# Kernel tuning notes

Measured on AMD Instinct MI355X. Metric: run time of the kernel, lower is better.

The kernel has to match this reference:

```python
import jax, jax.numpy as jnp
import numpy as np

B, N, C, H = 4, 1024, 1024, 16
D = C // H  # head_dim = 64


def _xavier(key, shape, gain):
    fan_in, fan_out = shape[1], shape[0]
    limit = gain * np.sqrt(6.0 / (fan_in + fan_out))
    return jax.random.uniform(key, shape, jnp.float32, -limit, limit)


def setup_inputs() -> dict:
    key = jax.random.key(0)
    ks = jax.random.split(key, 12)
    g = 2.0 ** (-0.5)
    return {
        "x": jax.random.normal(ks[0], (B, N, C), jnp.float32),
        "attn_bias": jax.random.normal(ks[1], (B, H, N, N), jnp.float32),
        "attn_mask": jnp.ones((B, N), jnp.int32),
        "Wq": _xavier(ks[2], (C, C), g), "bq": jnp.zeros((C,), jnp.float32),
        "Wk": _xavier(ks[3], (C, C), g), "bk": jnp.zeros((C,), jnp.float32),
        "Wv": _xavier(ks[4], (C, C), g), "bv": jnp.zeros((C,), jnp.float32),
        "Wo": _xavier(ks[5], (C, C), 1.0), "bo": jnp.zeros((C,), jnp.float32),
    }


def reference(x, attn_bias, attn_mask, Wq, bq, Wk, bk, Wv, bv, Wo, bo):
    scale = D ** (-0.5)
    # projections; nn.Linear computes x @ W.T + b
    def proj(W, b):
        return (x @ W.T + b).reshape(B, N, H, D).transpose(0, 2, 1, 3)  # [B,H,N,D]
    q = proj(Wq, bq) * scale
    k = proj(Wk, bk)
    v = proj(Wv, bv)
    scores = jnp.einsum("bhnd,bhmd->bhnm", q, k)  # [B,H,N,N]
    scores = scores + attn_bias  # attn_bias_type == 'add'
    # 2D mask [B,N] -> [B,1,1,N]; masked_fill where mask == 0
    mask = attn_mask[:, None, None, :]
    scores = jnp.where(mask == 0, -jnp.inf, scores)
    weights = jax.nn.softmax(scores, axis=-1)  # stable (internal max subtract)
    # attn_drop is identity in eval / p=0.0
    out = jnp.einsum("bhnm,bhmd->bhnd", weights, v)
    out = out.transpose(0, 2, 1, 3).reshape(B, N, C)
    return out @ Wo.T + bo
```

## Files before the change

kernel.cpp:

```cpp
#include <hip/hip_runtime.h>
#include <hip/hip_bf16.h>

#define B_ 4
#define N_ 1024
#define C_ 1024
#define H_ 16
#define D_ 64

typedef __attribute__((ext_vector_type(8))) short bf16x8;
typedef __attribute__((ext_vector_type(4))) float f32x4;

__device__ __forceinline__ void gld_lds16(const void* g, void* l) {
    __builtin_amdgcn_global_load_lds(
        (const __attribute__((address_space(1))) void*)g,
        (__attribute__((address_space(3))) void*)l, 16, 0, 0);
}

__global__ __launch_bounds__(256) void f2b_kernel(const float* __restrict__ s,
                                                  __hip_bfloat16* __restrict__ d,
                                                  int n) {
    int i = (blockIdx.x * 256 + threadIdx.x) * 4;
    if (i < n) {
        float4 v = *(const float4*)&s[i];
        d[i + 0] = __float2bfloat16(v.x);
        d[i + 1] = __float2bfloat16(v.y);
        d[i + 2] = __float2bfloat16(v.z);
        d[i + 3] = __float2bfloat16(v.w);
    }
}

__global__ __launch_bounds__(256) void f2b4_kernel(const float* __restrict__ w0,
                                                   const float* __restrict__ w1,
                                                   const float* __restrict__ w2,
                                                   const float* __restrict__ w3,
                                                   __hip_bfloat16* __restrict__ d0,
                                                   __hip_bfloat16* __restrict__ d1,
                                                   __hip_bfloat16* __restrict__ d2,
                                                   __hip_bfloat16* __restrict__ d3) {
    int sel = blockIdx.y;
    const float* s = sel == 0 ? w0 : sel == 1 ? w1 : sel == 2 ? w2 : w3;
    __hip_bfloat16* d = sel == 0 ? d0 : sel == 1 ? d1 : sel == 2 ? d2 : d3;
    int i = (blockIdx.x * 256 + threadIdx.x) * 4;
    float4 v = *(const float4*)&s[i];
    d[i + 0] = __float2bfloat16(v.x);
    d[i + 1] = __float2bfloat16(v.y);
    d[i + 2] = __float2bfloat16(v.z);
    d[i + 3] = __float2bfloat16(v.w);
}

__global__ __launch_bounds__(256) void gemm_qkv(const __hip_bfloat16* __restrict__ A,
                                                const __hip_bfloat16* __restrict__ wq,
                                                const __hip_bfloat16* __restrict__ wk,
                                                const __hip_bfloat16* __restrict__ wv,
                                                const float* __restrict__ bq,
                                                const float* __restrict__ bk,
                                                const float* __restrict__ bv,
                                                __hip_bfloat16* __restrict__ qo,
                                                __hip_bfloat16* __restrict__ ko,
                                                __hip_bfloat16* __restrict__ vto) {
    __shared__ __hip_bfloat16 Al[128 * 32];
    __shared__ __hip_bfloat16 Bl[128 * 32];
    const int sel = blockIdx.x >> 3;
    const __hip_bfloat16* Bw = sel == 0 ? wq : sel == 1 ? wk : wv;
    const float* bias = sel == 0 ? bq : sel == 1 ? bk : bv;
    const int t = threadIdx.x, w = t >> 6, l = t & 63;
    const int wr = w >> 1, wc = w & 1, lr = l & 15, lg = l >> 4;
    const int m0 = blockIdx.y * 128, n0 = (blockIdx.x & 7) * 128;
    const int K = C_;

    f32x4 acc[4][4] = {};

    for (int k0 = 0; k0 < K; k0 += 32) {
#pragma unroll
        for (int it = 0; it < 2; ++it) {
            int i = t + it * 256;
            int r = i >> 2, c8 = (i & 3) * 8;
            gld_lds16(A + (size_t)(m0 + r) * K + k0 + c8, &Al[i * 8]);
            gld_lds16(Bw + (size_t)(n0 + r) * K + k0 + c8, &Bl[i * 8]);
        }
        __syncthreads();
        bf16x8 af[4], bfr[4];
#pragma unroll
        for (int mi = 0; mi < 4; ++mi)
            af[mi] = *(const bf16x8*)&Al[(wr * 64 + mi * 16 + lr) * 32 + lg * 8];
#pragma unroll
        for (int ni = 0; ni < 4; ++ni)
            bfr[ni] = *(const bf16x8*)&Bl[(wc * 64 + ni * 16 + lr) * 32 + lg * 8];
#pragma unroll
        for (int mi = 0; mi < 4; ++mi)
#pragma unroll
            for (int ni = 0; ni < 4; ++ni)
                acc[mi][ni] = __builtin_amdgcn_mfma_f32_16x16x32_bf16(
                    af[mi], bfr[ni], acc[mi][ni], 0, 0, 0);
        __syncthreads();
    }

#pragma unroll
    for (int mi = 0; mi < 4; ++mi) {
#pragma unroll
        for (int ni = 0; ni < 4; ++ni) {
            int col = n0 + wc * 64 + ni * 16 + lr;
            float bb = bias[col];
#pragma unroll
            for (int j = 0; j < 4; ++j) {
                int row = m0 + wr * 64 + mi * 16 + lg * 4 + j;
                float v = acc[mi][ni][j] + bb;
                int bb_ = row >> 10, nn = row & 1023;
                int hh = col >> 6, dd = col & 63;
                if (sel == 0) {
                    qo[(((size_t)bb_ * H_ + hh) * N_ + nn) * D_ + dd] =
                        __float2bfloat16(v * 0.125f);
                } else if (sel == 1) {
                    ko[(((size_t)bb_ * H_ + hh) * N_ + nn) * D_ + dd] =
                        __float2bfloat16(v);
                } else {
                    vto[(((size_t)bb_ * H_ + hh) * D_ + dd) * N_ + nn] =
                        __float2bfloat16(v);
                }
            }
        }
    }
}

__global__ __launch_bounds__(256) void gemm_out(const __hip_bfloat16* __restrict__ A,
                                                const __hip_bfloat16* __restrict__ Bw,
                                                const float* __restrict__ bias,
                                                float* __restrict__ out) {
    __shared__ __hip_bfloat16 Al[128 * 32];
    __shared__ __hip_bfloat16 Bl[128 * 32];
    const int t = threadIdx.x, w = t >> 6, l = t & 63;
    const int wr = w >> 1, wc = w & 1, lr = l & 15, lg = l >> 4;
    const int m0 = blockIdx.y * 128, n0 = blockIdx.x * 128;
    const int K = C_;

    f32x4 acc[4][4] = {};

    for (int k0 = 0; k0 < K; k0 += 32) {
#pragma unroll
        for (int it = 0; it < 2; ++it) {
            int i = t + it * 256;
            int r = i >> 2, c8 = (i & 3) * 8;
            gld_lds16(A + (size_t)(m0 + r) * K + k0 + c8, &Al[i * 8]);
            gld_lds16(Bw + (size_t)(n0 + r) * K + k0 + c8, &Bl[i * 8]);
        }
        __syncthreads();
        bf16x8 af[4], bfr[4];
#pragma unroll
        for (int mi = 0; mi < 4; ++mi)
            af[mi] = *(const bf16x8*)&Al[(wr * 64 + mi * 16 + lr) * 32 + lg * 8];
#pragma unroll
        for (int ni = 0; ni < 4; ++ni)
            bfr[ni] = *(const bf16x8*)&Bl[(wc * 64 + ni * 16 + lr) * 32 + lg * 8];
#pragma unroll
        for (int mi = 0; mi < 4; ++mi)
#pragma unroll
            for (int ni = 0; ni < 4; ++ni)
                acc[mi][ni] = __builtin_amdgcn_mfma_f32_16x16x32_bf16(
                    af[mi], bfr[ni], acc[mi][ni], 0, 0, 0);
        __syncthreads();
    }

#pragma unroll
    for (int mi = 0; mi < 4; ++mi)
#pragma unroll
        for (int ni = 0; ni < 4; ++ni) {
            int col = n0 + wc * 64 + ni * 16 + lr;
            float bb = bias[col];
#pragma unroll
            for (int j = 0; j < 4; ++j) {
                int row = m0 + wr * 64 + mi * 16 + lg * 4 + j;
                out[(size_t)row * C_ + col] = acc[mi][ni][j] + bb;
            }
        }
}

#define ATTN_ITER(KT, CB, SB, BCUR, BNXT)                                          \
    {                                                                              \
        const int ktn_ = (KT) < 15 ? (KT) + 1 : 15;                                \
        gld_lds16(kg0 + (size_t)ktn_ * 4096, &Kl[SB][(w * 64) * 8]);               \
        gld_lds16(vg0 + ktn_ * 64, &Vl[SB][(w * 64) * 8]);                         \
        _Pragma("unroll")                                                          \
        for (int nkb = 0; nkb < 4; ++nkb)                                          \
            BNXT[nkb] = *(const f32x4*)&brow[ktn_ * 64 + nkb * 16 + lg * 4];       \
        __builtin_amdgcn_sched_barrier(0);                                         \
        asm volatile("s_waitcnt vmcnt(6)" ::: "memory");                           \
        __builtin_amdgcn_sched_barrier(0);                                         \
        __builtin_amdgcn_s_barrier();                                              \
        __builtin_amdgcn_sched_barrier(0);                                         \
        const __hip_bfloat16* Kb = &Kl[CB][0];                                     \
        float s[4][4];                                                             \
        __builtin_amdgcn_s_setprio(1);                                             \
        _Pragma("unroll")                                                          \
        for (int nkb = 0; nkb < 4; ++nkb) {                                        \
            f32x4 a = {};                                                          \
            _Pragma("unroll")                                                      \
            for (int half = 0; half < 2; ++half) {                                 \
                bf16x8 kf = *(const bf16x8*)                                       \
                    &Kb[(nkb * 16 + lr) * 64 + ((half * 32 + lg * 8) ^ swz)];      \
                a = __builtin_amdgcn_mfma_f32_16x16x32_bf16(kf, qf[half], a,       \
                                                            0, 0, 0);              \
            }                                                                      \
            f32x4 pen = *(const f32x4*)&Pen[(KT) * 64 + nkb * 16 + lg * 4];        \
            _Pragma("unroll")                                                      \
            for (int j = 0; j < 4; ++j) s[nkb][j] = a[j] + BCUR[nkb][j] + pen[j];  \
        }                                                                          \
        __builtin_amdgcn_s_setprio(0);                                             \
        float tm = s[0][0];                                                        \
        _Pragma("unroll")                                                          \
        for (int nkb = 0; nkb < 4; ++nkb)                                          \
            _Pragma("unroll")                                                      \
            for (int j = 0; j < 4; ++j) tm = fmaxf(tm, s[nkb][j]);                 \
        tm = fmaxf(tm, __shfl_xor(tm, 16));                                        \
        tm = fmaxf(tm, __shfl_xor(tm, 32));                                        \
        const float mn = fmaxf(m_, tm);                                            \
        const float al = __expf(m_ - mn);                                          \
        m_ = mn;                                                                   \
        float ts = 0.f;                                                            \
        _Pragma("unroll")                                                          \
        for (int nkb = 0; nkb < 4; ++nkb)                                          \
            _Pragma("unroll")                                                      \
            for (int j = 0; j < 4; ++j) {                                          \
                float p = __expf(s[nkb][j] - mn);                                  \
                s[nkb][j] = p;                                                     \
                ts += p;                                                           \
            }                                                                      \
        ts += __shfl_xor(ts, 16);                                                  \
        ts += __shfl_xor(ts, 32);                                                  \
        l_ = l_ * al + ts;                                                         \
        _Pragma("unroll")                                                          \
        for (int nkb = 0; nkb < 4; ++nkb) {                                        \
            __hip_bfloat16 pk[4];                                                  \
            _Pragma("unroll")                                                      \
            for (int j = 0; j < 4; ++j) pk[j] = __float2bfloat16(s[nkb][j]);       \
            *(short4*)&Pl[w][lr][nkb * 16 + lg * 4] = *(const short4*)pk;          \
        }                                                                          \
        float alr[4];                                                              \
        _Pragma("unroll")                                                          \
        for (int j = 0; j < 4; ++j) alr[j] = __shfl(al, lg * 4 + j);               \
        _Pragma("unroll")                                                          \
        for (int db = 0; db < 4; ++db)                                             \
            _Pragma("unroll")                                                      \
            for (int j = 0; j < 4; ++j) acc[db][j] *= alr[j];                      \
        const __hip_bfloat16* Vb = &Vl[CB][0];                                     \
        bf16x8 paf[2];                                                             \
        paf[0] = *(const bf16x8*)&Pl[w][lr][lg * 8];                               \
        paf[1] = *(const bf16x8*)&Pl[w][lr][32 + lg * 8];                          \
        __builtin_amdgcn_s_setprio(1);                                             \
        _Pragma("unroll")                                                          \
        for (int db = 0; db < 4; ++db)                                             \
            _Pragma("unroll")                                                      \
            for (int mh = 0; mh < 2; ++mh) {                                       \
                bf16x8 vf = *(const bf16x8*)                                       \
                    &Vb[(db * 16 + lr) * 64 + ((mh * 32 + lg * 8) ^ swz)];         \
                acc[db] = __builtin_amdgcn_mfma_f32_16x16x32_bf16(paf[mh], vf,     \
                                                                  acc[db], 0, 0,  \
                                                                  0);              \
            }                                                                      \
        __builtin_amdgcn_s_setprio(0);                                             \
        __builtin_amdgcn_sched_barrier(0);                                         \
        __builtin_amdgcn_s_barrier();                                              \
        __builtin_amdgcn_sched_barrier(0);                                         \
    }

__global__ __launch_bounds__(512, 4) void attn_kernel(const __hip_bfloat16* __restrict__ q,
                                                      const __hip_bfloat16* __restrict__ k,
                                                      const __hip_bfloat16* __restrict__ vt,
                                                      const float* __restrict__ bias,
                                                      const int* __restrict__ mask,
                                                      __hip_bfloat16* __restrict__ ao) {
    const int orig = blockIdx.x;
    const int wg = (orig & 7) * 64 + (orig >> 3);
    const int qt = wg & 7, h = (wg >> 3) & 15, b = wg >> 7;
    const int t = threadIdx.x, w = t >> 6, l = t & 63;
    const int lr = l & 15, lg = l >> 4;

    __shared__ __hip_bfloat16 Kl[2][64 * 64];
    __shared__ __hip_bfloat16 Vl[2][64 * 64];
    __shared__ float Pen[1024];
    __shared__ __hip_bfloat16 Pl[8][16][72];

    const size_t bh = (size_t)b * H_ + h;
    const int qr0 = qt * 128;
    const int myrow = qr0 + w * 16 + lr;
    const int orow_base = qr0 + w * 16 + lg * 4;

    {
        int2 mi = *(const int2*)&mask[b * N_ + t * 2];
        float2 p;
        p.x = mi.x ? 0.f : -1e30f;
        p.y = mi.y ? 0.f : -1e30f;
        *(float2*)&Pen[t * 2] = p;
    }
    __syncthreads();

    const int r0 = t >> 3;
    const int e0 = ((t & 7) * 8) ^ ((r0 & 7) << 3);
    const __hip_bfloat16* kg0 = k + (bh * N_ + r0) * D_ + e0;
    const __hip_bfloat16* vg0 = vt + (bh * D_ + r0) * N_ + e0;

    bf16x8 qf[2];
#pragma unroll
    for (int half = 0; half < 2; ++half)
        qf[half] = *(const bf16x8*)&q[(bh * N_ + myrow) * D_ + half * 32 + lg * 8];

    const float* brow = bias + ((size_t)bh * N_ + myrow) * N_;
    const int swz = (lr & 7) << 3;

    f32x4 acc[4] = {};
    float m_ = -3e38f, l_ = 0.f;

    __builtin_amdgcn_sched_barrier(0);
    gld_lds16(kg0, &Kl[0][(w * 64) * 8]);
    gld_lds16(vg0, &Vl[0][(w * 64) * 8]);
    f32x4 bA[4], bB[4];
#pragma unroll
    for (int nkb = 0; nkb < 4; ++nkb)
        bA[nkb] = *(const f32x4*)&brow[nkb * 16 + lg * 4];
    __builtin_amdgcn_sched_barrier(0);

    for (int kt = 0; kt < 16; kt += 2) {
        ATTN_ITER(kt, 0, 1, bA, bB);
        ATTN_ITER(kt + 1, 1, 0, bB, bA);
    }

    float dummy = bA[0][0] + bA[1][0] + bA[2][0] + bA[3][0];
    asm volatile("" :: "v"(dummy));

    float linv[4];
#pragma unroll
    for (int j = 0; j < 4; ++j) linv[j] = 1.f / __shfl(l_, lg * 4 + j);
#pragma unroll
    for (int db = 0; db < 4; ++db)
#pragma unroll
        for (int j = 0; j < 4; ++j)
            ao[((size_t)b * N_ + orow_base + j) * C_ + h * 64 + db * 16 + lr] =
                __float2bfloat16(acc[db][j] * linv[j]);
}

extern "C" void kernel_launch(void* const* d_in, const int* in_sizes, int n_in,
                              void* d_out, int out_size, void* d_ws, size_t ws_size,
                              hipStream_t stream) {
    const float* x    = (const float*)d_in[0];
    const float* bias = (const float*)d_in[1];
    const int*   mask = (const int*)d_in[2];
    const float* Wq   = (const float*)d_in[3];
    const float* bq   = (const float*)d_in[4];
    const float* Wk   = (const float*)d_in[5];
    const float* bk   = (const float*)d_in[6];
    const float* Wv   = (const float*)d_in[7];
    const float* bv   = (const float*)d_in[8];
    const float* Wo   = (const float*)d_in[9];
    const float* bo   = (const float*)d_in[10];
    float* out = (float*)d_out;

    char* ws = (char*)d_ws;
    const size_t MB = 1u << 20;
    __hip_bfloat16* xb  = (__hip_bfloat16*)(ws + 0 * MB);
    __hip_bfloat16* wqb = (__hip_bfloat16*)(ws + 8 * MB);
    __hip_bfloat16* wkb = (__hip_bfloat16*)(ws + 10 * MB);
    __hip_bfloat16* wvb = (__hip_bfloat16*)(ws + 12 * MB);
    __hip_bfloat16* wob = (__hip_bfloat16*)(ws + 14 * MB);
    __hip_bfloat16* qb  = (__hip_bfloat16*)(ws + 16 * MB);
    __hip_bfloat16* kb  = (__hip_bfloat16*)(ws + 24 * MB);
    __hip_bfloat16* vtb = (__hip_bfloat16*)(ws + 32 * MB);
    __hip_bfloat16* aob = (__hip_bfloat16*)(ws + 40 * MB);

    f2b_kernel<<<4096, 256, 0, stream>>>(x, xb, B_ * N_ * C_);
    f2b4_kernel<<<dim3(1024, 4), 256, 0, stream>>>(Wq, Wk, Wv, Wo, wqb, wkb, wvb, wob);

    gemm_qkv<<<dim3(24, 32), 256, 0, stream>>>(xb, wqb, wkb, wvb, bq, bk, bv, qb, kb, vtb);

    attn_kernel<<<512, 512, 0, stream>>>(qb, kb, vtb, bias, mask, aob);

    gemm_out<<<dim3(8, 32), 256, 0, stream>>>(aob, wob, bo, out);
}
```

Measured before the change: 158.8 us.

## Shrink attention blocks to 64 query rows and pass P via shuffles instead of LDS

The attention kernel now launches 1024 workgroups of 256 threads, each covering 64 query rows, so every thread issues two K/V global-to-LDS loads per tile. The probability matrix is packed with v_cvt_pk_bf16_f32 and rearranged into the MFMA A-operand layout using cross-lane shuffles, replacing the Pl LDS round trip. This removes LDS traffic and shared memory for P and changes occupancy and grid shape, but K/V tiles are reloaded twice as often per query row and the extra shuffles add VALU work.

```diff
diff --git a/kernel.cpp b/kernel.cpp
--- a/kernel.cpp
+++ b/kernel.cpp
@@ -9,11 +9,18 @@
 
 typedef __attribute__((ext_vector_type(8))) short bf16x8;
 typedef __attribute__((ext_vector_type(4))) float f32x4;
+typedef __attribute__((ext_vector_type(4))) int i32x4;
 
 __device__ __forceinline__ void gld_lds16(const void* g, void* l) {
     __builtin_amdgcn_global_load_lds(
         (const __attribute__((address_space(1))) void*)g,
         (__attribute__((address_space(3))) void*)l, 16, 0, 0);
+}
+
+__device__ __forceinline__ unsigned cvt_pk_bf16(float lo, float hi) {
+    unsigned r;
+    asm("v_cvt_pk_bf16_f32 %0, %1, %2" : "=v"(r) : "v"(lo), "v"(hi));
+    return r;
 }
 
 __global__ __launch_bounds__(256) void f2b_kernel(const float* __restrict__ s,
@@ -178,12 +185,14 @@
     {                                                                              \
         const int ktn_ = (KT) < 15 ? (KT) + 1 : 15;                                \
         gld_lds16(kg0 + (size_t)ktn_ * 4096, &Kl[SB][(w * 64) * 8]);               \
+        gld_lds16(kg1 + (size_t)ktn_ * 4096, &Kl[SB][(256 + w * 64) * 8]);         \
         gld_lds16(vg0 + ktn_ * 64, &Vl[SB][(w * 64) * 8]);                         \
+        gld_lds16(vg1 + ktn_ * 64, &Vl[SB][(256 + w * 64) * 8]);                   \
         _Pragma("unroll")                                                          \
         for (int nkb = 0; nkb < 4; ++nkb)                                          \
             BNXT[nkb] = *(const f32x4*)&brow[ktn_ * 64 + nkb * 16 + lg * 4];       \
         __builtin_amdgcn_sched_barrier(0);                                         \
-        asm volatile("s_waitcnt vmcnt(6)" ::: "memory");                           \
+        asm volatile("s_waitcnt vmcnt(8)" ::: "memory");                           \
         __builtin_amdgcn_sched_barrier(0);                                         \
         __builtin_amdgcn_s_barrier();                                              \
         __builtin_amdgcn_sched_barrier(0);                                         \
@@ -227,12 +236,11 @@
         ts += __shfl_xor(ts, 16);                                                  \
         ts += __shfl_xor(ts, 32);                                                  \
         l_ = l_ * al + ts;                                                         \
+        unsigned pk0[4], pk1[4];                                                   \
         _Pragma("unroll")                                                          \
         for (int nkb = 0; nkb < 4; ++nkb) {                                        \
-            __hip_bfloat16 pk[4];                                                  \
-            _Pragma("unroll")                                                      \
-            for (int j = 0; j < 4; ++j) pk[j] = __float2bfloat16(s[nkb][j]);       \
-            *(short4*)&Pl[w][lr][nkb * 16 + lg * 4] = *(const short4*)pk;          \
+            pk0[nkb] = cvt_pk_bf16(s[nkb][0], s[nkb][1]);                          \
+            pk1[nkb] = cvt_pk_bf16(s[nkb][2], s[nkb][3]);                          \
         }                                                                          \
         float alr[4];                                                              \
         _Pragma("unroll")                                                          \
@@ -242,61 +250,75 @@
             _Pragma("unroll")                                                      \
             for (int j = 0; j < 4; ++j) acc[db][j] *= alr[j];                      \
         const __hip_bfloat16* Vb = &Vl[CB][0];                                     \
-        bf16x8 paf[2];                                                             \
-        paf[0] = *(const bf16x8*)&Pl[w][lr][lg * 8];                               \
-        paf[1] = *(const bf16x8*)&Pl[w][lr][32 + lg * 8];                          \
         __builtin_amdgcn_s_setprio(1);                                             \
         _Pragma("unroll")                                                          \
-        for (int db = 0; db < 4; ++db)                                             \
-            _Pragma("unroll")                                                      \
-            for (int mh = 0; mh < 2; ++mh) {                                       \
+        for (int mh = 0; mh < 2; ++mh) {                                           \
+            const int n0_ = 2 * mh, n1_ = 2 * mh + 1;                              \
+            int e0a = __shfl((int)pk0[n0_], shi0), e0b = __shfl((int)pk0[n1_], shi0); \
+            int e1a = __shfl((int)pk1[n0_], shi0), e1b = __shfl((int)pk1[n1_], shi0); \
+            int e2a = __shfl((int)pk0[n0_], shi1), e2b = __shfl((int)pk0[n1_], shi1); \
+            int e3a = __shfl((int)pk1[n0_], shi1), e3b = __shfl((int)pk1[n1_], shi1); \
+            i32x4 pw;                                                              \
+            pw[0] = lghi ? e0b : e0a;                                              \
+            pw[1] = lghi ? e1b : e1a;                                              \
+            pw[2] = lghi ? e2b : e2a;                                              \
+            pw[3] = lghi ? e3b : e3a;                                              \
+            bf16x8 paf = *(bf16x8*)&pw;                                            \
+            _Pragma("unroll")                                                      \
+            for (int db = 0; db < 4; ++db) {                                       \
                 bf16x8 vf = *(const bf16x8*)                                       \
                     &Vb[(db * 16 + lr) * 64 + ((mh * 32 + lg * 8) ^ swz)];         \
-                acc[db] = __builtin_amdgcn_mfma_f32_16x16x32_bf16(paf[mh], vf,     \
+                acc[db] = __builtin_amdgcn_mfma_f32_16x16x32_bf16(paf, vf,         \
                                                                   acc[db], 0, 0,  \
                                                                   0);              \
             }                                                                      \
+        }                                                                          \
         __builtin_amdgcn_s_setprio(0);                                             \
         __builtin_amdgcn_sched_barrier(0);                                         \
         __builtin_amdgcn_s_barrier();                                              \
         __builtin_amdgcn_sched_barrier(0);                                         \
     }
 
-__global__ __launch_bounds__(512, 4) void attn_kernel(const __hip_bfloat16* __restrict__ q,
+__global__ __launch_bounds__(256, 4) void attn_kernel(const __hip_bfloat16* __restrict__ q,
                                                       const __hip_bfloat16* __restrict__ k,
                                                       const __hip_bfloat16* __restrict__ vt,
                                                       const float* __restrict__ bias,
                                                       const int* __restrict__ mask,
                                                       __hip_bfloat16* __restrict__ ao) {
     const int orig = blockIdx.x;
-    const int wg = (orig & 7) * 64 + (orig >> 3);
-    const int qt = wg & 7, h = (wg >> 3) & 15, b = wg >> 7;
+    const int wg = (orig & 7) * 128 + (orig >> 3);
+    const int qt = wg & 15, h = (wg >> 4) & 15, b = wg >> 8;
     const int t = threadIdx.x, w = t >> 6, l = t & 63;
     const int lr = l & 15, lg = l >> 4;
 
     __shared__ __hip_bfloat16 Kl[2][64 * 64];
     __shared__ __hip_bfloat16 Vl[2][64 * 64];
     __shared__ float Pen[1024];
-    __shared__ __hip_bfloat16 Pl[8][16][72];
 
     const size_t bh = (size_t)b * H_ + h;
-    const int qr0 = qt * 128;
+    const int qr0 = qt * 64;
     const int myrow = qr0 + w * 16 + lr;
     const int orow_base = qr0 + w * 16 + lg * 4;
 
     {
-        int2 mi = *(const int2*)&mask[b * N_ + t * 2];
-        float2 p;
+        int4 mi = *(const int4*)&mask[b * N_ + t * 4];
+        float4 p;
         p.x = mi.x ? 0.f : -1e30f;
         p.y = mi.y ? 0.f : -1e30f;
-        *(float2*)&Pen[t * 2] = p;
+        p.z = mi.z ? 0.f : -1e30f;
+        p.w = mi.w ? 0.f : -1e30f;
+        *(float4*)&Pen[t * 4] = p;
     }
     __syncthreads();
 
-    const int r0 = t >> 3;
-    const int e0 = ((t & 7) * 8) ^ ((r0 & 7) << 3);
+    const int c0 = t, c1 = t + 256;
+    const int r0 = c0 >> 3, r1 = c1 >> 3;
+    const int e0 = ((c0 & 7) * 8) ^ ((r0 & 7) << 3);
+    const int e1 = ((c1 & 7) * 8) ^ ((r1 & 7) << 3);
     const __hip_bfloat16* kg0 = k + (bh * N_ + r0) * D_ + e0;
+    const __hip_bfloat16* kg1 = k + (bh * N_ + r1) * D_ + e1;
     const __hip_bfloat16* vg0 = vt + (bh * D_ + r0) * N_ + e0;
+    const __hip_bfloat16* vg1 = vt + (bh * D_ + r1) * N_ + e1;
 
     bf16x8 qf[2];
 #pragma unroll
@@ -305,13 +327,18 @@
 
     const float* brow = bias + ((size_t)bh * N_ + myrow) * N_;
     const int swz = (lr & 7) << 3;
+    const int shi0 = ((lg & 1) << 5) + lr;
+    const int shi1 = shi0 + 16;
+    const bool lghi = (lg >> 1) != 0;
 
     f32x4 acc[4] = {};
     float m_ = -3e38f, l_ = 0.f;
 
     __builtin_amdgcn_sched_barrier(0);
     gld_lds16(kg0, &Kl[0][(w * 64) * 8]);
+    gld_lds16(kg1, &Kl[0][(256 + w * 64) * 8]);
     gld_lds16(vg0, &Vl[0][(w * 64) * 8]);
+    gld_lds16(vg1, &Vl[0][(256 + w * 64) * 8]);
     f32x4 bA[4], bB[4];
 #pragma unroll
     for (int nkb = 0; nkb < 4; ++nkb)
@@ -370,7 +397,7 @@
 
     gemm_qkv<<<dim3(24, 32), 256, 0, stream>>>(xb, wqb, wkb, wvb, bq, bk, bv, qb, kb, vtb);
 
-    attn_kernel<<<512, 512, 0, stream>>>(qb, kb, vtb, bias, mask, aob);
+    attn_kernel<<<1024, 256, 0, stream>>>(qb, kb, vtb, bias, mask, aob);
 
     gemm_out<<<dim3(8, 32), 256, 0, stream>>>(aob, wob, bo, out);
 }
```

Result: slower. 165.5 us (+4.2%).
